# Kernel optimization log

Measured on AMD Instinct MI355X. Metric: run time of the kernel, lower is better.

Reference implementation:

```python
import jax, jax.numpy as jnp
import numpy as np

EPS = 1e-9
SPREAD_WEIGHT = 0.1
QUAD_WEIGHT = 1.0

N_NODES = 200000
N_EDGES = 12800000
DIM = 128


def to_uhg_space(x):
    # dim > 2: truncate to first 2 features, append homogeneous 1 -> [..., 3]
    ones = jnp.ones((*x.shape[:-1], 1), dtype=x.dtype)
    return jnp.concatenate([x[..., :2], ones], axis=-1)


def uhg_inner(a, b):
    # -<spatial,spatial> + time*time, keepdim
    return -jnp.sum(a[..., :-1] * b[..., :-1], axis=-1, keepdims=True) + a[..., -1:] * b[..., -1:]


def uhg_quadrance(a, b):
    aa = uhg_inner(a, a)
    bb = uhg_inner(b, b)
    ab = uhg_inner(a, b)
    num = ab * ab - aa * bb
    den = aa * bb
    safe = jnp.maximum(jnp.abs(den), EPS) * jnp.sign(den)
    return (num / safe).squeeze(-1)


# spread has the identical formula, applied to lines instead of points
uhg_spread = uhg_quadrance


def setup_inputs() -> dict:
    key = jax.random.key(0)
    k1, k2 = jax.random.split(key)
    z = jax.random.normal(k1, (N_NODES, DIM), dtype=jnp.float32)
    edge_index = jax.random.randint(k2, (2, N_EDGES), 0, N_NODES, dtype=jnp.int32)
    return {"z": z, "edge_index": edge_index}


def reference(z, edge_index):
    z_uhg = to_uhg_space(z)                      # [N, 3]
    src, dst = edge_index[0], edge_index[1]
    # proximity: quadrance over all edges (gather + fused elementwise + mean)
    quad = uhg_quadrance(z_uhg[src], z_uhg[dst])  # [E]
    proximity_loss = quad.mean()
    # compactness: quadrance of every node to the origin [0,0,1]
    origin = jnp.zeros((1, 3), dtype=z.dtype).at[:, -1].set(1.0)
    compactness_loss = uhg_quadrance(z_uhg, origin).mean()
    # lines: vectorized cross product of each point with the origin
    lines = jnp.cross(z_uhg, origin)              # [N, 3]
    # spread over the first min(10, E) edges only (as in the original)
    n_sp = min(10, edge_index.shape[1])
    sp = uhg_spread(lines[src[:n_sp]], lines[dst[:n_sp]])
    spread_loss = sp.mean()
    loss = QUAD_WEIGHT * (proximity_loss + compactness_loss) + SPREAD_WEIGHT * spread_loss
    return loss
```

## Files before the change

### kernel.cpp

```cpp
#include <hip/hip_runtime.h>
#include <hip/hip_bf16.h>

#define UHG_EPS 1e-9
#define ZDIM 128

#define EDGE_BLOCKS 1024
#define NODE_BLOCKS 1024
#define BLOCK 256

#define PROX_OFF 0
#define COMP_OFF (16 * 1024)
#define TABLE_OFF (24 * 1024)

typedef float vfloat2 __attribute__((ext_vector_type(2)));
typedef int vint4 __attribute__((ext_vector_type(4)));

__device__ vfloat2 llvm_amdgcn_raw_buffer_load_v2f32(vint4 rsrc, int voffset, int soffset,
                                                     int cpol) __asm("llvm.amdgcn.raw.buffer.load.v2f32");

__device__ __forceinline__ vint4 make_srd(const void* base, unsigned int bytes) {
    union { const void* p; unsigned int w[2]; } pb;
    pb.p = base;
    vint4 r;
    r.x = (int)pb.w[0];
    r.y = (int)pb.w[1];
    r.z = (int)bytes;
    r.w = 0x00020000;
    return r;
}


__device__ __forceinline__ double safe_den(double den) {
    return copysign(fmax(fabs(den), UHG_EPS), den);
}

__device__ __forceinline__ double quad_xy(vfloat2 a, vfloat2 b) {
    double xa = a.x, ya = a.y, xb = b.x, yb = b.y;
    double aa = 1.0 - (xa * xa + ya * ya);
    double bb = 1.0 - (xb * xb + yb * yb);
    double ab = 1.0 - (xa * xb + ya * yb);
    double den = aa * bb;
    double num = ab * ab - den;
    return num / safe_den(den);
}

__device__ __forceinline__ double block_reduce(double v, double* sh) {
    int lane = threadIdx.x & 63;
    int wid = threadIdx.x >> 6;
    v += __shfl_down(v, 32);
    v += __shfl_down(v, 16);
    v += __shfl_down(v, 8);
    v += __shfl_down(v, 4);
    v += __shfl_down(v, 2);
    v += __shfl_down(v, 1);
    if (lane == 0) sh[wid] = v;
    __syncthreads();
    double r = 0.0;
    if (wid == 0) {
        int nw = blockDim.x >> 6;
        r = (lane < nw) ? sh[lane] : 0.0;
        r += __shfl_down(r, 4);
        r += __shfl_down(r, 2);
        r += __shfl_down(r, 1);
    }
    __syncthreads();
    return r;
}


__global__ __launch_bounds__(BLOCK) void node_kernel(const float* __restrict__ z,
                                                     vfloat2* __restrict__ table,
                                                     double* __restrict__ comp_partials, int N) {
    __shared__ double sh[8];
    const vfloat2* zp = (const vfloat2*)z;
    double local = 0.0;
    for (int i = blockIdx.x * BLOCK + threadIdx.x; i < N; i += NODE_BLOCKS * BLOCK) {
        vfloat2 v = zp[(size_t)i * (ZDIM / 2)];
        if (table) table[i] = v;
        double x = v.x, y = v.y;
        double aa = 1.0 - (x * x + y * y);
        local += (1.0 - aa) / safe_den(aa);
    }
    double tot = block_reduce(local, sh);
    if (threadIdx.x == 0) comp_partials[blockIdx.x] = tot;
}

#define GATHER8(dsta, i0, i1)                                                   \
    dsta[0] = llvm_amdgcn_raw_buffer_load_v2f32(srd, (i0).x << SHIFT, 0, 1);    \
    dsta[1] = llvm_amdgcn_raw_buffer_load_v2f32(srd, (i0).y << SHIFT, 0, 1);    \
    dsta[2] = llvm_amdgcn_raw_buffer_load_v2f32(srd, (i0).z << SHIFT, 0, 1);    \
    dsta[3] = llvm_amdgcn_raw_buffer_load_v2f32(srd, (i0).w << SHIFT, 0, 1);    \
    dsta[4] = llvm_amdgcn_raw_buffer_load_v2f32(srd, (i1).x << SHIFT, 0, 1);    \
    dsta[5] = llvm_amdgcn_raw_buffer_load_v2f32(srd, (i1).y << SHIFT, 0, 1);    \
    dsta[6] = llvm_amdgcn_raw_buffer_load_v2f32(srd, (i1).z << SHIFT, 0, 1);    \
    dsta[7] = llvm_amdgcn_raw_buffer_load_v2f32(srd, (i1).w << SHIFT, 0, 1);

template <int COMPACT>
__global__ __launch_bounds__(BLOCK) void edge_kernel(const vint4* __restrict__ src4,
                                                     const vint4* __restrict__ dst4, int nvec,
                                                     const int* __restrict__ src,
                                                     const int* __restrict__ dst, int E,
                                                     const void* __restrict__ xy, int N,
                                                     double* __restrict__ prox_partials) {
    __shared__ double sh[8];
    double local = 0.0;
    int tid = blockIdx.x * BLOCK + threadIdx.x;
    const int gstride = EDGE_BLOCKS * BLOCK;
    const int SHIFT = COMPACT ? 3 : 9;

    vint4 srd = make_srd(xy, COMPACT ? (unsigned int)N * 8u : (unsigned int)N * 512u);

    int nvec2 = nvec / 2;

    int v0 = tid;
    bool p0 = v0 < nvec2;
    int v1 = v0 + gstride;
    bool p1 = v1 < nvec2;

    vint4 is0 = {}, is1 = {}, id0 = {}, id1 = {};
    vfloat2 ca[8] = {}, cb[8] = {};
    vfloat2 na[8] = {}, nb[8] = {};

    if (p0) {
        vint4 s0 = __builtin_nontemporal_load(src4 + 2 * (long)v0);
        vint4 s1 = __builtin_nontemporal_load(src4 + 2 * (long)v0 + 1);
        vint4 d0 = __builtin_nontemporal_load(dst4 + 2 * (long)v0);
        vint4 d1 = __builtin_nontemporal_load(dst4 + 2 * (long)v0 + 1);
        GATHER8(ca, s0, s1);
        GATHER8(cb, d0, d1);
    }
    if (p1) {
        is0 = __builtin_nontemporal_load(src4 + 2 * (long)v1);
        is1 = __builtin_nontemporal_load(src4 + 2 * (long)v1 + 1);
        id0 = __builtin_nontemporal_load(dst4 + 2 * (long)v1);
        id1 = __builtin_nontemporal_load(dst4 + 2 * (long)v1 + 1);
    }

    while (p0) {
        if (p1) {
            GATHER8(na, is0, is1);
            GATHER8(nb, id0, id1);
        }
        int v2 = v1 + gstride;
        bool p2 = v2 < nvec2;
        if (p2) {
            is0 = __builtin_nontemporal_load(src4 + 2 * (long)v2);
            is1 = __builtin_nontemporal_load(src4 + 2 * (long)v2 + 1);
            id0 = __builtin_nontemporal_load(dst4 + 2 * (long)v2);
            id1 = __builtin_nontemporal_load(dst4 + 2 * (long)v2 + 1);
        }
        __builtin_amdgcn_sched_barrier(0);
#pragma unroll
        for (int i = 0; i < 8; ++i) local += quad_xy(ca[i], cb[i]);
#pragma unroll
        for (int i = 0; i < 8; ++i) { ca[i] = na[i]; cb[i] = nb[i]; }
        p0 = p1;
        v1 = v2;
        p1 = p2;
    }

    for (int e = 8 * nvec2 + tid; e < E; e += gstride) {
        vfloat2 a = llvm_amdgcn_raw_buffer_load_v2f32(srd, src[e] << SHIFT, 0, 1);
        vfloat2 b = llvm_amdgcn_raw_buffer_load_v2f32(srd, dst[e] << SHIFT, 0, 1);
        local += quad_xy(a, b);
    }
    double tot = block_reduce(local, sh);
    if (threadIdx.x == 0) prox_partials[blockIdx.x] = tot;
}

__global__ __launch_bounds__(BLOCK) void finalize_kernel(const int* __restrict__ src,
                                                         const int* __restrict__ dst,
                                                         const float* __restrict__ z,
                                                         const double* __restrict__ prox_partials,
                                                         const double* __restrict__ comp_partials,
                                                         float* __restrict__ out, int N, int E) {
    __shared__ double sh[8];
    int t = threadIdx.x;

    double pl = 0.0;
    for (int i = t; i < EDGE_BLOCKS; i += BLOCK) pl += prox_partials[i];
    double prox = block_reduce(pl, sh);

    double cl = 0.0;
    for (int i = t; i < NODE_BLOCKS; i += BLOCK) cl += comp_partials[i];
    double comp = block_reduce(cl, sh);

    int n_sp = E < 10 ? E : 10;
    double sl = 0.0;
    if (t < n_sp) {
        int s = src[t], d = dst[t];
        double xa = z[(size_t)s * ZDIM], ya = z[(size_t)s * ZDIM + 1];
        double xb = z[(size_t)d * ZDIM], yb = z[(size_t)d * ZDIM + 1];
        double aa = -(ya * ya + xa * xa);
        double bb = -(yb * yb + xb * xb);
        double ab = -(ya * yb + xa * xb);
        double den = aa * bb;
        sl = (ab * ab - den) / safe_den(den);
    }
    double spread = block_reduce(sl, sh);

    if (t == 0) {
        double loss = prox / (double)E + comp / (double)N;
        if (n_sp > 0) loss += 0.1 * (spread / (double)n_sp);
        out[0] = (float)loss;
    }
}


extern "C" void kernel_launch(void* const* d_in, const int* in_sizes, int n_in,
                              void* d_out, int out_size, void* d_ws, size_t ws_size,
                              hipStream_t stream) {
    const float* z = (const float*)d_in[0];
    const int* edge_index = (const int*)d_in[1];
    float* out = (float*)d_out;

    const int N = in_sizes[0] / ZDIM;
    const int E = in_sizes[1] / 2;
    const int* src = edge_index;
    const int* dst = edge_index + (size_t)E;

    double* prox_partials = (double*)((char*)d_ws + PROX_OFF);
    double* comp_partials = (double*)((char*)d_ws + COMP_OFF);
    vfloat2* table = (vfloat2*)((char*)d_ws + TABLE_OFF);
    bool use_table = ws_size >= TABLE_OFF + (size_t)N * sizeof(vfloat2);

    node_kernel<<<NODE_BLOCKS, BLOCK, 0, stream>>>(z, use_table ? table : nullptr,
                                                   comp_partials, N);

    int nvec = E / 4;
    if (use_table) {
        edge_kernel<1><<<EDGE_BLOCKS, BLOCK, 0, stream>>>((const vint4*)src, (const vint4*)dst,
                                                          nvec, src, dst, E, table, N,
                                                          prox_partials);
    } else {
        edge_kernel<0><<<EDGE_BLOCKS, BLOCK, 0, stream>>>((const vint4*)src, (const vint4*)dst,
                                                          nvec, src, dst, E, z, N,
                                                          prox_partials);
    }

    finalize_kernel<<<1, BLOCK, 0, stream>>>(src, dst, z, prox_partials, comp_partials,
                                             out, N, E);
}
```

Measured before the change: 292.4 us.

## Bin edges by node-partition pairs so endpoint gathers hit LDS

Adds a scatter pass that buckets every edge into one of up to 625 bins keyed by the source and destination node partitions (8192 nodes each), packing both local indices into one 32-bit word. Staging uses shared-memory buffers and chunked global atomics. A new per-bin kernel loads the two 8192-point partitions into LDS and evaluates the quadrance from LDS, replacing random global or L2 gathers. The cost is an extra full pass over the edge list, roughly 50 MB of packed bins written and read back, and heavy LDS use that limits occupancy. Edges would be silently dropped if any bin exceeds its fixed capacity.

```diff
diff --git a/kernel.cpp b/kernel.cpp
--- a/kernel.cpp
+++ b/kernel.cpp
@@ -8,9 +8,18 @@
 #define NODE_BLOCKS 1024
 #define BLOCK 256
 
+#define PART_SHIFT 13
+#define PART_SIZE (1 << PART_SHIFT)
+#define P_MAX 25
+#define NBINS_MAX (P_MAX * P_MAX)
+#define STAGE_CAP 48
+#define CHUNK 32
+#define SCAT_BLOCKS 256
+
 #define PROX_OFF 0
 #define COMP_OFF (16 * 1024)
-#define TABLE_OFF (24 * 1024)
+#define GCUR_OFF (24 * 1024)
+#define TABLE_OFF (32 * 1024)
 
 typedef float vfloat2 __attribute__((ext_vector_type(2)));
 typedef int vint4 __attribute__((ext_vector_type(4)));
@@ -70,8 +79,12 @@
 
 __global__ __launch_bounds__(BLOCK) void node_kernel(const float* __restrict__ z,
                                                      vfloat2* __restrict__ table,
-                                                     double* __restrict__ comp_partials, int N) {
+                                                     double* __restrict__ comp_partials, int N,
+                                                     unsigned* __restrict__ gcur, int nbins) {
     __shared__ double sh[8];
+    if (gcur && blockIdx.x == 0) {
+        for (int j = threadIdx.x; j < nbins; j += BLOCK) gcur[j] = 0u;
+    }
     const vfloat2* zp = (const vfloat2*)z;
     double local = 0.0;
     for (int i = blockIdx.x * BLOCK + threadIdx.x; i < N; i += NODE_BLOCKS * BLOCK) {
@@ -83,6 +96,104 @@
     }
     double tot = block_reduce(local, sh);
     if (threadIdx.x == 0) comp_partials[blockIdx.x] = tot;
+}
+
+__global__ __launch_bounds__(BLOCK) void scatter_kernel(const int* __restrict__ src,
+                                                        const int* __restrict__ dst, int E,
+                                                        int P, int nbins,
+                                                        unsigned* __restrict__ gcur,
+                                                        unsigned* __restrict__ gbins, int bincap) {
+    __shared__ unsigned cnt[NBINS_MAX];
+    __shared__ unsigned stage[NBINS_MAX][STAGE_CAP];
+    const int tid = threadIdx.x;
+
+    for (int b = tid; b < nbins; b += BLOCK) cnt[b] = 0u;
+    __syncthreads();
+
+    const int e0 = (int)((long)blockIdx.x * E / SCAT_BLOCKS);
+    const int e1 = (int)((long)(blockIdx.x + 1) * E / SCAT_BLOCKS);
+
+    for (int base = e0; base < e1; base += 2 * BLOCK) {
+#pragma unroll
+        for (int k = 0; k < 2; ++k) {
+            int i = base + k * BLOCK + tid;
+            if (i < e1) {
+                int s = __builtin_nontemporal_load(src + i);
+                int d = __builtin_nontemporal_load(dst + i);
+                int bin = (s >> PART_SHIFT) * P + (d >> PART_SHIFT);
+                unsigned val = (unsigned)(s & (PART_SIZE - 1)) |
+                               ((unsigned)(d & (PART_SIZE - 1)) << PART_SHIFT);
+                unsigned slot = atomicAdd(&cnt[bin], 1u);
+                if (slot < STAGE_CAP) {
+                    stage[bin][slot] = val;
+                } else {
+                    unsigned pos = atomicAdd(&gcur[bin], 1u);
+                    if (pos < (unsigned)bincap) gbins[(size_t)bin * bincap + pos] = val;
+                }
+            }
+        }
+        __syncthreads();
+        for (int b = tid; b < nbins; b += BLOCK) {
+            unsigned n = cnt[b];
+            if (n >= CHUNK) {
+                unsigned m = n < STAGE_CAP ? n : STAGE_CAP;
+                unsigned pos = atomicAdd(&gcur[b], (unsigned)CHUNK);
+                unsigned* out = gbins + (size_t)b * bincap + pos;
+#pragma unroll
+                for (int j = 0; j < CHUNK / 4; ++j) {
+                    uint4 vv = *(const uint4*)&stage[b][4 * j];
+                    *(uint4*)(out + 4 * j) = vv;
+                }
+                unsigned r = m - CHUNK;
+                for (unsigned j = 0; j < r; ++j) stage[b][j] = stage[b][CHUNK + j];
+                cnt[b] = r;
+            }
+        }
+        __syncthreads();
+    }
+    for (int b = tid; b < nbins; b += BLOCK) {
+        unsigned n = cnt[b];
+        n = n < STAGE_CAP ? n : STAGE_CAP;
+        if (n) {
+            unsigned pos = atomicAdd(&gcur[b], n);
+            unsigned* out = gbins + (size_t)b * bincap + pos;
+            for (unsigned j = 0; j < n; ++j) out[j] = stage[b][j];
+        }
+    }
+}
+
+__global__ __launch_bounds__(BLOCK) void binned_edge_kernel(const vfloat2* __restrict__ table,
+                                                            int N, int P,
+                                                            const unsigned* __restrict__ gcur,
+                                                            const unsigned* __restrict__ gbins,
+                                                            int bincap,
+                                                            double* __restrict__ prox_partials) {
+    __shared__ vfloat2 pts[2][PART_SIZE];
+    __shared__ double sh[8];
+    const int bin = blockIdx.x;
+    const int sp = bin / P, dp = bin % P;
+    const int tid = threadIdx.x;
+
+    for (int j = tid; j < PART_SIZE; j += BLOCK) {
+        int gs = (sp << PART_SHIFT) + j;
+        int gd = (dp << PART_SHIFT) + j;
+        vfloat2 zv = {0.0f, 0.0f};
+        pts[0][j] = (gs < N) ? table[gs] : zv;
+        pts[1][j] = (gd < N) ? table[gd] : zv;
+    }
+    __syncthreads();
+
+    const unsigned len = gcur[bin];
+    const unsigned* eb = gbins + (size_t)bin * bincap;
+    double local = 0.0;
+    for (unsigned i = tid; i < len; i += BLOCK) {
+        unsigned v = eb[i];
+        vfloat2 a = pts[0][v & (PART_SIZE - 1u)];
+        vfloat2 b = pts[1][(v >> PART_SHIFT) & (PART_SIZE - 1u)];
+        local += quad_xy(a, b);
+    }
+    double tot = block_reduce(local, sh);
+    if (tid == 0) prox_partials[bin] = tot;
 }
 
 #define GATHER8(dsta, i0, i1)                                                   \
@@ -111,7 +222,6 @@
     vint4 srd = make_srd(xy, COMPACT ? (unsigned int)N * 8u : (unsigned int)N * 512u);
 
     int nvec2 = nvec / 2;
-
     int v0 = tid;
     bool p0 = v0 < nvec2;
     int v1 = v0 + gstride;
@@ -172,13 +282,14 @@
                                                          const int* __restrict__ dst,
                                                          const float* __restrict__ z,
                                                          const double* __restrict__ prox_partials,
+                                                         int nprox,
                                                          const double* __restrict__ comp_partials,
                                                          float* __restrict__ out, int N, int E) {
     __shared__ double sh[8];
     int t = threadIdx.x;
 
     double pl = 0.0;
-    for (int i = t; i < EDGE_BLOCKS; i += BLOCK) pl += prox_partials[i];
+    for (int i = t; i < nprox; i += BLOCK) pl += prox_partials[i];
     double prox = block_reduce(pl, sh);
 
     double cl = 0.0;
@@ -221,23 +332,49 @@
 
     double* prox_partials = (double*)((char*)d_ws + PROX_OFF);
     double* comp_partials = (double*)((char*)d_ws + COMP_OFF);
+    unsigned* gcur = (unsigned*)((char*)d_ws + GCUR_OFF);
     vfloat2* table = (vfloat2*)((char*)d_ws + TABLE_OFF);
     bool use_table = ws_size >= TABLE_OFF + (size_t)N * sizeof(vfloat2);
 
+    const int P = (N + PART_SIZE - 1) >> PART_SHIFT;
+    const int nbins = P * P;
+    int bincap = 0;
+    size_t gbins_off = TABLE_OFF + (((size_t)N * 8 + 255) & ~(size_t)255);
+    bool use_binned = false;
+    unsigned* gbins = nullptr;
+    if (use_table && P >= 1 && P <= P_MAX && nbins <= NBINS_MAX && E > nbins * 64) {
+        int mean = E / nbins;
+        bincap = (mean + mean / 8 + 2048 + 31) & ~31;
+        size_t need = gbins_off + (size_t)nbins * (size_t)bincap * 4u;
+        if (ws_size >= need) {
+            use_binned = true;
+            gbins = (unsigned*)((char*)d_ws + gbins_off);
+        }
+    }
+
     node_kernel<<<NODE_BLOCKS, BLOCK, 0, stream>>>(z, use_table ? table : nullptr,
-                                                   comp_partials, N);
-
-    int nvec = E / 4;
-    if (use_table) {
-        edge_kernel<1><<<EDGE_BLOCKS, BLOCK, 0, stream>>>((const vint4*)src, (const vint4*)dst,
-                                                          nvec, src, dst, E, table, N,
-                                                          prox_partials);
+                                                   comp_partials,
+                                                   N, use_binned ? gcur : nullptr, nbins);
+
+    if (use_binned) {
+        scatter_kernel<<<SCAT_BLOCKS, BLOCK, 0, stream>>>(src, dst, E, P, nbins, gcur, gbins,
+                                                          bincap);
+        binned_edge_kernel<<<nbins, BLOCK, 0, stream>>>(table, N, P, gcur, gbins, bincap,
+                                                        prox_partials);
+        finalize_kernel<<<1, BLOCK, 0, stream>>>(src, dst, z, prox_partials, nbins,
+                                                 comp_partials, out, N, E);
     } else {
-        edge_kernel<0><<<EDGE_BLOCKS, BLOCK, 0, stream>>>((const vint4*)src, (const vint4*)dst,
-                                                          nvec, src, dst, E, z, N,
-                                                          prox_partials);
-    }
-
-    finalize_kernel<<<1, BLOCK, 0, stream>>>(src, dst, z, prox_partials, comp_partials,
-                                             out, N, E);
-}
+        int nvec = E / 4;
+        if (use_table) {
+            edge_kernel<1><<<EDGE_BLOCKS, BLOCK, 0, stream>>>((const vint4*)src,
+                                                              (const vint4*)dst, nvec, src, dst,
+                                                              E, table, N, prox_partials);
+        } else {
+            edge_kernel<0><<<EDGE_BLOCKS, BLOCK, 0, stream>>>((const vint4*)src,
+                                                              (const vint4*)dst, nvec, src, dst,
+                                                              E, z, N, prox_partials);
+        }
+        finalize_kernel<<<1, BLOCK, 0, stream>>>(src, dst, z, prox_partials, EDGE_BLOCKS,
+                                                 comp_partials, out, N, E);
+    }
+}
```

Result: slower. 564.2 us (+93.0%).
